# Kernel tuning notes

Hardware: AMD Instinct MI355X
Metric: run time of the kernel (lower is better)

The kernel has to match this reference:

```python
import jax, jax.numpy as jnp
import numpy as np

B, S, E, A = 4, 2048, 1024, 64  # batch, seq, embedding_size, attention_size


def setup_inputs() -> dict:
    key = jax.random.key(0)
    k1, k2 = jax.random.split(key)
    embedding = jax.random.normal(k1, (B, S, E), dtype=jnp.float32)
    # nn.Linear(embedding_size, attention_size, bias=False).weight has shape [A, E]
    Wk = jax.random.normal(k2, (A, E), dtype=jnp.float32) * (1.0 / np.sqrt(E))
    return {"embedding": embedding, "Wk": Wk}


def reference(embedding, Wk):
    # NOTE: the original module (buggily) calls self.key() for q, k, AND v.
    # We reproduce that math faithfully: q = k = v = embedding @ Wk.T.
    k = jnp.einsum('bse,ae->bsa', embedding, Wk)  # [B,S,A]
    q = k
    v = k
    x = jnp.einsum('bqa,bka->bqk', q, k) / jnp.sqrt(jnp.float32(A))  # [B,S,S]
    # Faithful to masked_fill(torch.tril(x) == 0, -inf): masks the strict upper
    # triangle (tril zeros it) plus any lower-triangle entries exactly equal to 0.
    x = jnp.where(jnp.tril(x) == 0, -jnp.inf, x)
    x = jax.nn.softmax(x, axis=2)
    return jnp.einsum('bqk,bka->bqa', x, v)  # [B,S,A]
```

## Files before the change

kernel.cpp:

```cpp
#include <hip/hip_runtime.h>
#include <math.h>

#define BATCH 4
#define SLEN  2048
#define EMB   1024
#define AH    64

typedef __attribute__((ext_vector_type(8))) short bf16x8;
typedef __attribute__((ext_vector_type(4))) float f32x4;

#define MFMA16(a, b, c) __builtin_amdgcn_mfma_f32_16x16x32_bf16((a), (b), (c), 0, 0, 0)

__device__ __forceinline__ void async16(const void* g, void* l) {
  __builtin_amdgcn_global_load_lds(
      (const __attribute__((address_space(1))) unsigned int*)g,
      (__attribute__((address_space(3))) unsigned int*)l, 16, 0, 0);
}

__device__ __forceinline__ short f2bf(float x) {
  union { float f; unsigned u; } v; v.f = x;
  unsigned r = v.u + 0x7fffu + ((v.u >> 16) & 1u);
  return (short)(r >> 16);
}
__device__ __forceinline__ float bf2f(short h) {
  union { unsigned u; float f; } v; v.u = ((unsigned)(unsigned short)h) << 16;
  return v.f;
}

__device__ __forceinline__ void split_trunc(float4 a0, float4 a1, bf16x8& hi, bf16x8& lo) {
  unsigned c[8] = {__float_as_uint(a0.x), __float_as_uint(a0.y), __float_as_uint(a0.z),
                   __float_as_uint(a0.w), __float_as_uint(a1.x), __float_as_uint(a1.y),
                   __float_as_uint(a1.z), __float_as_uint(a1.w)};
  union { bf16x8 v; unsigned d[4]; } H, L;
  H.d[0] = __builtin_amdgcn_perm(c[1], c[0], 0x07060302u);
  H.d[1] = __builtin_amdgcn_perm(c[3], c[2], 0x07060302u);
  H.d[2] = __builtin_amdgcn_perm(c[5], c[4], 0x07060302u);
  H.d[3] = __builtin_amdgcn_perm(c[7], c[6], 0x07060302u);
  unsigned e[8];
#pragma unroll
  for (int j = 0; j < 8; ++j)
    e[j] = __float_as_uint(__uint_as_float(c[j]) - __uint_as_float(c[j] & 0xffff0000u));
  L.d[0] = __builtin_amdgcn_perm(e[1], e[0], 0x07060302u);
  L.d[1] = __builtin_amdgcn_perm(e[3], e[2], 0x07060302u);
  L.d[2] = __builtin_amdgcn_perm(e[5], e[4], 0x07060302u);
  L.d[3] = __builtin_amdgcn_perm(e[7], e[6], 0x07060302u);
  hi = H.v; lo = L.v;
}

__device__ __forceinline__ int slot_off(int qt) {
  return (qt == 0) ? 0 : qt + (((qt - 1) * (qt - 1)) >> 2);
}

#define CH_SHORTS 24576


__global__ __launch_bounds__(256) void prep_wk_kernel(const float* __restrict__ Wk,
                                                      short* __restrict__ BpkG) {
  int tg = blockIdx.x * 256 + threadIdx.x;
  int kc = tg >> 8, rem = tg & 255, nt = rem >> 6, lane = rem & 63;
  int n = nt * 16 + (lane & 15);
  int k = kc * 32 + (lane >> 4) * 8;
  const float* src = Wk + (size_t)n * EMB + k;
  float4 a0 = *(const float4*)src;
  float4 a1 = *(const float4*)(src + 4);
  bf16x8 hi, lo;
  split_trunc(a0, a1, hi, lo);
  short* dst = BpkG + ((size_t)(kc * 4 + nt) * 128 + lane) * 8;
  *(bf16x8*)dst = hi;
  *(bf16x8*)(dst + 512) = lo;
}

__global__ __launch_bounds__(256) void gemm_k_kernel(const float* __restrict__ emb,
                                                     const short* __restrict__ BpkG,
                                                     short* __restrict__ Kpack) {
  __shared__ __align__(16) float eT[16384];

  const int t = threadIdx.x;
  const int w = t >> 6, l = t & 63, lm = l & 15, quad = l >> 4;
  const int nt = w;
  const int row0 = blockIdx.x * 16;

  {
    int rowl = 4 * w + (l >> 4);
    int du = (l & 15) ^ (rowl & 7);
    const float* src = emb + (size_t)(row0 + rowl) * EMB + du * 4;
#pragma unroll
    for (int s = 0; s < 16; ++s)
      async16(src + s * 64, eT + s * 1024 + w * 256);
  }
  __syncthreads();

  f32x4 acc = {0.f, 0.f, 0.f, 0.f};
#pragma unroll
  for (int s = 0; s < 16; ++s) {
    const char* eS = (const char*)(eT + s * 1024);
    const short* bg = BpkG + (size_t)s * 8192;
#pragma unroll
    for (int kc = 0; kc < 2; ++kc) {
      int du0 = kc * 8 + quad * 2;
      float4 a0 = *(const float4*)(eS + lm * 256 + ((du0) ^ (lm & 7)) * 16);
      float4 a1 = *(const float4*)(eS + lm * 256 + ((du0 + 1) ^ (lm & 7)) * 16);
      bf16x8 ahi, alo;
      split_trunc(a0, a1, ahi, alo);
      bf16x8 bhi = *(const bf16x8*)(bg + (((kc * 4 + nt) * 2 + 0) * 64 + l) * 8);
      bf16x8 blo = *(const bf16x8*)(bg + (((kc * 4 + nt) * 2 + 1) * 64 + l) * 8);
      acc = MFMA16(ahi, bhi, acc);
      acc = MFMA16(ahi, blo, acc);
      acc = MFMA16(alo, bhi, acc);
    }
  }

  const int a = nt * 16 + lm;
#pragma unroll
  for (int r = 0; r < 4; ++r) {
    int srow = row0 + quad * 4 + r;
    float v = acc[r];
    short h = f2bf(v);
    short lo2 = f2bf(v - bf2f(h));
    int bb = srow >> 11, si = srow & 2047, c = si >> 7, key = si & 127;
    int kb = key >> 4, klm = key & 15;
    size_t cb = (size_t)(bb * 16 + c) * CH_SHORTS;
    size_t kbo = (size_t)((kb * 2 + (a >> 5)) * 64 + ((a & 31) >> 3) * 16 + klm) * 8 + (a & 7);
    Kpack[cb + kbo] = h;
    Kpack[cb + 8192 + kbo] = lo2;
    size_t vbo = (size_t)(((key >> 5) * 4 + (a >> 4)) * 64 + ((key & 31) >> 3) * 16 + (a & 15)) * 8 + (key & 7);
    Kpack[cb + 16384 + vbo] = h;
  }
}

__global__ __launch_bounds__(256, 3) void flash_kernel(const short* __restrict__ Kpack,
                                                       short* __restrict__ OpartH,
                                                       float2* __restrict__ mlpart) {
  const int c = blockIdx.x, qt = blockIdx.y, b = blockIdx.z;
  if (2 * c > qt) return;

  __shared__ __align__(16) short KLs[16384];
  __shared__ __align__(16) short Plds[4][16][132];

  const int t = threadIdx.x;
  const int w = t >> 6, l = t & 63, lm = l & 15, quad = l >> 4;
  const int k0 = c * 128;
  const int qr0 = qt * 64 + w * 16;

  const short* chunkG = Kpack + (size_t)(b * 16 + c) * CH_SHORTS;
#pragma unroll
  for (int u = 0; u < 8; ++u) {
    int slot = w * 8 + u;
    async16(chunkG + slot * 512 + l * 8, KLs + slot * 512);
  }

  const short* qG = Kpack + (size_t)(b * 16 + (qt >> 1)) * CH_SHORTS + ((qt & 1) * 4 + w) * 1024;
  bf16x8 qh0 = *(const bf16x8*)(qG + l * 8);
  bf16x8 qh1 = *(const bf16x8*)(qG + 512 + l * 8);
  bf16x8 ql0 = *(const bf16x8*)(qG + 8192 + l * 8);
  bf16x8 ql1 = *(const bf16x8*)(qG + 8192 + 512 + l * 8);

  bf16x8 vf[4][4];
#pragma unroll
  for (int kc2 = 0; kc2 < 4; ++kc2)
#pragma unroll
    for (int nt = 0; nt < 4; ++nt)
      vf[kc2][nt] = *(const bf16x8*)(chunkG + 16384 + ((kc2 * 4 + nt) * 64 + l) * 8);

  __syncthreads();

  f32x4 sc[8];
#pragma unroll
  for (int kg = 0; kg < 8; ++kg) {
    bf16x8 bh0 = *(const bf16x8*)(KLs + ((kg * 2 + 0) * 64 + l) * 8);
    bf16x8 bh1 = *(const bf16x8*)(KLs + ((kg * 2 + 1) * 64 + l) * 8);
    bf16x8 bl0 = *(const bf16x8*)(KLs + 8192 + ((kg * 2 + 0) * 64 + l) * 8);
    bf16x8 bl1 = *(const bf16x8*)(KLs + 8192 + ((kg * 2 + 1) * 64 + l) * 8);
    f32x4 s = {0.f, 0.f, 0.f, 0.f};
    s = MFMA16(qh0, bh0, s);
    s = MFMA16(qh0, bl0, s);
    s = MFMA16(ql0, bh0, s);
    s = MFMA16(qh1, bh1, s);
    s = MFMA16(qh1, bl1, s);
    s = MFMA16(ql1, bh1, s);
    sc[kg] = s;
  }

  float rm[4] = {-INFINITY, -INFINITY, -INFINITY, -INFINITY};
#pragma unroll
  for (int kg = 0; kg < 8; ++kg) {
    const int col = k0 + kg * 16 + lm;
#pragma unroll
    for (int r = 0; r < 4; ++r) {
      const int row = qr0 + quad * 4 + r;
      float v = sc[kg][r] * 0.125f;
      v = (col > row || v == 0.0f) ? -INFINITY : v;
      sc[kg][r] = v;
      rm[r] = fmaxf(rm[r], v);
    }
  }
  float m_i[4], l_i[4];
#pragma unroll
  for (int r = 0; r < 4; ++r) {
    for (int off = 1; off < 16; off <<= 1) rm[r] = fmaxf(rm[r], __shfl_xor(rm[r], off, 16));
    m_i[r] = rm[r];
  }
  float rs[4] = {0.f, 0.f, 0.f, 0.f};
#pragma unroll
  for (int kg = 0; kg < 8; ++kg)
#pragma unroll
    for (int r = 0; r < 4; ++r) {
      float p = (sc[kg][r] == -INFINITY) ? 0.f : __expf(sc[kg][r] - m_i[r]);
      sc[kg][r] = p;
      rs[r] += p;
    }
#pragma unroll
  for (int r = 0; r < 4; ++r) {
    for (int off = 1; off < 16; off <<= 1) rs[r] += __shfl_xor(rs[r], off, 16);
    l_i[r] = rs[r];
  }

#pragma unroll
  for (int kg = 0; kg < 8; ++kg)
#pragma unroll
    for (int r = 0; r < 4; ++r)
      Plds[w][quad * 4 + r][kg * 16 + lm] = f2bf(sc[kg][r]);

  f32x4 o[4] = {{0.f,0.f,0.f,0.f},{0.f,0.f,0.f,0.f},{0.f,0.f,0.f,0.f},{0.f,0.f,0.f,0.f}};
#pragma unroll
  for (int kc2 = 0; kc2 < 4; ++kc2) {
    bf16x8 pf = *(const bf16x8*)&Plds[w][lm][kc2 * 32 + quad * 8];
#pragma unroll
    for (int nt = 0; nt < 4; ++nt)
      o[nt] = MFMA16(pf, vf[kc2][nt], o[nt]);
  }

  const int slot = b * 272 + slot_off(qt) + c;
  short* Ob = OpartH + (size_t)slot * 4096;
#pragma unroll
  for (int nt = 0; nt < 4; ++nt)
#pragma unroll
    for (int r = 0; r < 4; ++r)
      Ob[(size_t)(w * 16 + quad * 4 + r) * AH + nt * 16 + lm] = f2bf(o[nt][r]);
  if (lm == 0) {
#pragma unroll
    for (int r = 0; r < 4; ++r)
      mlpart[(size_t)slot * 64 + w * 16 + quad * 4 + r] = make_float2(m_i[r], l_i[r]);
  }
}

__global__ __launch_bounds__(256) void merge_kernel(const short* __restrict__ OpartH,
                                                    const float2* __restrict__ mlpart,
                                                    float* __restrict__ out) {
  __shared__ __align__(16) short ldsO[16 * 1024];
  __shared__ float wtab[16][17];
  const int t = threadIdx.x;
  const int w = t >> 6, l = t & 63;
  const int rg = blockIdx.x, qt = blockIdx.y, b = blockIdx.z;
  const int r0 = rg * 16;
  const int nch = (qt >> 1) + 1;
  const int slotbase = b * 272 + slot_off(qt);

#pragma unroll
  for (int u = 0; u < 8; ++u) {
    int idx = w * 8 + u;
    int c = idx >> 1, half = idx & 1;
    if (c < nch)
      async16(OpartH + (size_t)(slotbase + c) * 4096 + r0 * 64 + half * 512 + l * 8,
              ldsO + c * 1024 + half * 512 + l * 8);
  }

  const int row = w * 4 + (l >> 4), c = l & 15;
  float mc = -INFINITY, lc = 0.f;
  if (c < nch) {
    float2 ml = mlpart[(size_t)(slotbase + c) * 64 + r0 + row];
    mc = ml.x; lc = ml.y;
  }
  float M = mc;
  for (int off = 1; off < 16; off <<= 1) M = fmaxf(M, __shfl_xor(M, off, 16));
  float wgt = (mc != -INFINITY) ? __expf(mc - M) : 0.f;
  float L = lc * wgt;
  for (int off = 1; off < 16; off <<= 1) L += __shfl_xor(L, off, 16);
  wtab[row][c] = wgt / L;

  __syncthreads();

  const int row2 = t >> 4, a0 = (t & 15) * 4;
  float4 acc = make_float4(0.f, 0.f, 0.f, 0.f);
  for (int cc = 0; cc < nch; ++cc) {
    float wv = wtab[row2][cc];
    short4 v4 = *(const short4*)(ldsO + cc * 1024 + row2 * 64 + a0);
    acc.x += wv * bf2f(v4.x); acc.y += wv * bf2f(v4.y);
    acc.z += wv * bf2f(v4.z); acc.w += wv * bf2f(v4.w);
  }
  *(float4*)&out[((size_t)(b * 2048 + qt * 64 + r0 + row2)) * AH + a0] = acc;
}

extern "C" void kernel_launch(void* const* d_in, const int* in_sizes, int n_in,
                              void* d_out, int out_size, void* d_ws, size_t ws_size,
                              hipStream_t stream) {
  const float* emb = (const float*)d_in[0];
  const float* Wk  = (const float*)d_in[1];
  float* out = (float*)d_out;
  char* ws = (char*)d_ws;

  short*  Kpack  = (short*)(ws);
  short*  BpkG   = (short*)(ws + 3145728);
  short*  OpartH = (short*)(ws + 3670016);
  float2* mlpart = (float2*)(ws + 12582912);

  prep_wk_kernel<<<dim3(32), dim3(256), 0, stream>>>(Wk, BpkG);
  gemm_k_kernel<<<dim3(512), dim3(256), 0, stream>>>(emb, BpkG, Kpack);
  flash_kernel<<<dim3(16, 32, 4), dim3(256), 0, stream>>>(Kpack, OpartH, mlpart);
  merge_kernel<<<dim3(4, 32, 4), dim3(256), 0, stream>>>(OpartH, mlpart, out);
}
```

Measured before the change: 105.5 us.

## Fuse split-K merge into flash kernel via last-block atomic counter

Drops the separate merge kernel launch. Each flash block bumps a per-(batch, query-tile) counter after writing its partial output. The last block to arrive for that tile then merges all chunk partials for its 64 rows, looping over four row groups and reusing a shared-memory union. The counters are reset in the prep kernel on every call. In exchange, the merge runs serially in the tail block of each tile. The counter uses a release-only atomic with no acquire fence, so partials written by other blocks may be read stale across the cache domains of different dies.

Result: slower. 158.2 us (+50.0%).

```diff
diff --git a/kernel.cpp b/kernel.cpp
--- a/kernel.cpp
+++ b/kernel.cpp
@@ -53,9 +53,13 @@
 
 #define CH_SHORTS 24576
 
+#define CNT(i) flags[(size_t)(i) << 4]
+
 
 __global__ __launch_bounds__(256) void prep_wk_kernel(const float* __restrict__ Wk,
-                                                      short* __restrict__ BpkG) {
+                                                      short* __restrict__ BpkG,
+                                                      int* __restrict__ flags) {
+  if (blockIdx.x == 0 && threadIdx.x < 128) CNT(threadIdx.x) = 0;
   int tg = blockIdx.x * 256 + threadIdx.x;
   int kc = tg >> 8, rem = tg & 255, nt = rem >> 6, lane = rem & 63;
   int n = nt * 16 + (lane & 15);
@@ -128,25 +132,33 @@
   }
 }
 
+union __align__(16) FMem {
+  struct { short KLs[16384]; short Plds[4][16][132]; } f;
+  struct { short ldsO[16384]; float wtab[16][17]; } m;
+};
+
 __global__ __launch_bounds__(256, 3) void flash_kernel(const short* __restrict__ Kpack,
                                                        short* __restrict__ OpartH,
-                                                       float2* __restrict__ mlpart) {
+                                                       float2* __restrict__ mlpart,
+                                                       float* __restrict__ out,
+                                                       int* __restrict__ flags) {
   const int c = blockIdx.x, qt = blockIdx.y, b = blockIdx.z;
   if (2 * c > qt) return;
 
-  __shared__ __align__(16) short KLs[16384];
-  __shared__ __align__(16) short Plds[4][16][132];
+  __shared__ FMem sm;
+  __shared__ int s_last;
 
   const int t = threadIdx.x;
   const int w = t >> 6, l = t & 63, lm = l & 15, quad = l >> 4;
   const int k0 = c * 128;
   const int qr0 = qt * 64 + w * 16;
+  const int nch = (qt >> 1) + 1;
 
   const short* chunkG = Kpack + (size_t)(b * 16 + c) * CH_SHORTS;
 #pragma unroll
   for (int u = 0; u < 8; ++u) {
     int slot = w * 8 + u;
-    async16(chunkG + slot * 512 + l * 8, KLs + slot * 512);
+    async16(chunkG + slot * 512 + l * 8, sm.f.KLs + slot * 512);
   }
 
   const short* qG = Kpack + (size_t)(b * 16 + (qt >> 1)) * CH_SHORTS + ((qt & 1) * 4 + w) * 1024;
@@ -167,10 +179,10 @@
   f32x4 sc[8];
 #pragma unroll
   for (int kg = 0; kg < 8; ++kg) {
-    bf16x8 bh0 = *(const bf16x8*)(KLs + ((kg * 2 + 0) * 64 + l) * 8);
-    bf16x8 bh1 = *(const bf16x8*)(KLs + ((kg * 2 + 1) * 64 + l) * 8);
-    bf16x8 bl0 = *(const bf16x8*)(KLs + 8192 + ((kg * 2 + 0) * 64 + l) * 8);
-    bf16x8 bl1 = *(const bf16x8*)(KLs + 8192 + ((kg * 2 + 1) * 64 + l) * 8);
+    bf16x8 bh0 = *(const bf16x8*)(sm.f.KLs + ((kg * 2 + 0) * 64 + l) * 8);
+    bf16x8 bh1 = *(const bf16x8*)(sm.f.KLs + ((kg * 2 + 1) * 64 + l) * 8);
+    bf16x8 bl0 = *(const bf16x8*)(sm.f.KLs + 8192 + ((kg * 2 + 0) * 64 + l) * 8);
+    bf16x8 bl1 = *(const bf16x8*)(sm.f.KLs + 8192 + ((kg * 2 + 1) * 64 + l) * 8);
     f32x4 s = {0.f, 0.f, 0.f, 0.f};
     s = MFMA16(qh0, bh0, s);
     s = MFMA16(qh0, bl0, s);
@@ -219,18 +231,19 @@
   for (int kg = 0; kg < 8; ++kg)
 #pragma unroll
     for (int r = 0; r < 4; ++r)
-      Plds[w][quad * 4 + r][kg * 16 + lm] = f2bf(sc[kg][r]);
+      sm.f.Plds[w][quad * 4 + r][kg * 16 + lm] = f2bf(sc[kg][r]);
 
   f32x4 o[4] = {{0.f,0.f,0.f,0.f},{0.f,0.f,0.f,0.f},{0.f,0.f,0.f,0.f},{0.f,0.f,0.f,0.f}};
 #pragma unroll
   for (int kc2 = 0; kc2 < 4; ++kc2) {
-    bf16x8 pf = *(const bf16x8*)&Plds[w][lm][kc2 * 32 + quad * 8];
+    bf16x8 pf = *(const bf16x8*)&sm.f.Plds[w][lm][kc2 * 32 + quad * 8];
 #pragma unroll
     for (int nt = 0; nt < 4; ++nt)
       o[nt] = MFMA16(pf, vf[kc2][nt], o[nt]);
   }
 
-  const int slot = b * 272 + slot_off(qt) + c;
+  const int slotbase = b * 272 + slot_off(qt);
+  const int slot = slotbase + c;
   short* Ob = OpartH + (size_t)slot * 4096;
 #pragma unroll
   for (int nt = 0; nt < 4; ++nt)
@@ -242,53 +255,51 @@
     for (int r = 0; r < 4; ++r)
       mlpart[(size_t)slot * 64 + w * 16 + quad * 4 + r] = make_float2(m_i[r], l_i[r]);
   }
-}
-
-__global__ __launch_bounds__(256) void merge_kernel(const short* __restrict__ OpartH,
-                                                    const float2* __restrict__ mlpart,
-                                                    float* __restrict__ out) {
-  __shared__ __align__(16) short ldsO[16 * 1024];
-  __shared__ float wtab[16][17];
-  const int t = threadIdx.x;
-  const int w = t >> 6, l = t & 63;
-  const int rg = blockIdx.x, qt = blockIdx.y, b = blockIdx.z;
-  const int r0 = rg * 16;
-  const int nch = (qt >> 1) + 1;
-  const int slotbase = b * 272 + slot_off(qt);
-
-#pragma unroll
-  for (int u = 0; u < 8; ++u) {
-    int idx = w * 8 + u;
-    int c = idx >> 1, half = idx & 1;
-    if (c < nch)
-      async16(OpartH + (size_t)(slotbase + c) * 4096 + r0 * 64 + half * 512 + l * 8,
-              ldsO + c * 1024 + half * 512 + l * 8);
-  }
-
-  const int row = w * 4 + (l >> 4), c = l & 15;
-  float mc = -INFINITY, lc = 0.f;
-  if (c < nch) {
-    float2 ml = mlpart[(size_t)(slotbase + c) * 64 + r0 + row];
-    mc = ml.x; lc = ml.y;
-  }
-  float M = mc;
-  for (int off = 1; off < 16; off <<= 1) M = fmaxf(M, __shfl_xor(M, off, 16));
-  float wgt = (mc != -INFINITY) ? __expf(mc - M) : 0.f;
-  float L = lc * wgt;
-  for (int off = 1; off < 16; off <<= 1) L += __shfl_xor(L, off, 16);
-  wtab[row][c] = wgt / L;
 
   __syncthreads();
-
-  const int row2 = t >> 4, a0 = (t & 15) * 4;
-  float4 acc = make_float4(0.f, 0.f, 0.f, 0.f);
-  for (int cc = 0; cc < nch; ++cc) {
-    float wv = wtab[row2][cc];
-    short4 v4 = *(const short4*)(ldsO + cc * 1024 + row2 * 64 + a0);
-    acc.x += wv * bf2f(v4.x); acc.y += wv * bf2f(v4.y);
-    acc.z += wv * bf2f(v4.z); acc.w += wv * bf2f(v4.w);
-  }
-  *(float4*)&out[((size_t)(b * 2048 + qt * 64 + r0 + row2)) * AH + a0] = acc;
+  if (t == 0)
+    s_last = (__hip_atomic_fetch_add(&CNT(b * 32 + qt), 1, __ATOMIC_RELEASE,
+                                     __HIP_MEMORY_SCOPE_AGENT) == nch - 1);
+  __syncthreads();
+  if (!s_last) return;
+
+  for (int rg = 0; rg < 4; ++rg) {
+    __syncthreads();
+    const int r0 = rg * 16;
+#pragma unroll
+    for (int u = 0; u < 8; ++u) {
+      int idx = w * 8 + u;
+      int cc = idx >> 1, half = idx & 1;
+      if (cc < nch)
+        async16(OpartH + (size_t)(slotbase + cc) * 4096 + r0 * 64 + half * 512 + l * 8,
+                sm.m.ldsO + cc * 1024 + half * 512 + l * 8);
+    }
+
+    const int row = w * 4 + (l >> 4), cw = l & 15;
+    float mc = -INFINITY, lc = 0.f;
+    if (cw < nch) {
+      float2 ml = mlpart[(size_t)(slotbase + cw) * 64 + r0 + row];
+      mc = ml.x; lc = ml.y;
+    }
+    float M = mc;
+    for (int off = 1; off < 16; off <<= 1) M = fmaxf(M, __shfl_xor(M, off, 16));
+    float wgt = (mc != -INFINITY) ? __expf(mc - M) : 0.f;
+    float L = lc * wgt;
+    for (int off = 1; off < 16; off <<= 1) L += __shfl_xor(L, off, 16);
+    sm.m.wtab[row][cw] = wgt / L;
+
+    __syncthreads();
+
+    const int row2 = t >> 4, a0 = (t & 15) * 4;
+    float4 acc = make_float4(0.f, 0.f, 0.f, 0.f);
+    for (int cc = 0; cc < nch; ++cc) {
+      float wv = sm.m.wtab[row2][cc];
+      short4 v4 = *(const short4*)(sm.m.ldsO + cc * 1024 + row2 * 64 + a0);
+      acc.x += wv * bf2f(v4.x); acc.y += wv * bf2f(v4.y);
+      acc.z += wv * bf2f(v4.z); acc.w += wv * bf2f(v4.w);
+    }
+    *(float4*)&out[((size_t)(b * 2048 + qt * 64 + r0 + row2)) * AH + a0] = acc;
+  }
 }
 
 extern "C" void kernel_launch(void* const* d_in, const int* in_sizes, int n_in,
@@ -303,9 +314,9 @@
   short*  BpkG   = (short*)(ws + 3145728);
   short*  OpartH = (short*)(ws + 3670016);
   float2* mlpart = (float2*)(ws + 12582912);
-
-  prep_wk_kernel<<<dim3(32), dim3(256), 0, stream>>>(Wk, BpkG);
+  int*    flags  = (int*)(ws + 13139968);
+
+  prep_wk_kernel<<<dim3(32), dim3(256), 0, stream>>>(Wk, BpkG, flags);
   gemm_k_kernel<<<dim3(512), dim3(256), 0, stream>>>(emb, BpkG, Kpack);
-  flash_kernel<<<dim3(16, 32, 4), dim3(256), 0, stream>>>(Kpack, OpartH, mlpart);
-  merge_kernel<<<dim3(4, 32, 4), dim3(256), 0, stream>>>(OpartH, mlpart, out);
-}
+  flash_kernel<<<dim3(16, 32, 4), dim3(256), 0, stream>>>(Kpack, OpartH, mlpart, out, flags);
+}
```
